# Optimization experiments

Hardware: AMD Instinct MI355X
Metric: run time of the kernel (lower is better)

## Reference

```python
import jax, jax.numpy as jnp
import numpy as np

N_NODES = 50000


def _cluster_gcn_conv(x, row, col, W_out, b_out, W_root, num_nodes):
    # PyG ClusterGCNConv with diag_lambda=0.0 and self-loops already added.
    deg = jax.ops.segment_sum(jnp.ones_like(col, dtype=x.dtype), col,
                              num_segments=num_nodes)
    deg_inv = 1.0 / jnp.clip(deg, 1.0)
    w = deg_inv[col]                       # [E_total]
    msg = x[row] * w[:, None]              # [E_total, d] gather + scale
    agg = jax.ops.segment_sum(msg, col, num_segments=num_nodes)  # scatter-add
    return agg @ W_out + b_out + x @ W_root


def setup_inputs() -> dict:
    key = jax.random.key(0)
    ks = jax.random.split(key, 12)
    N, E, d_in, d_h, d_out = N_NODES, 800000, 128, 128, 64
    x = jax.random.normal(ks[0], (N, d_in), dtype=jnp.float32)
    edge_index = jax.random.randint(ks[1], (2, E), 0, N, dtype=jnp.int64)
    s = lambda fan_in: 1.0 / np.sqrt(fan_in)
    return {
        "x": x,
        "edge_index": edge_index,
        "W1_out": jax.random.normal(ks[2], (d_in, d_h), jnp.float32) * s(d_in),
        "b1": jnp.zeros((d_h,), jnp.float32),
        "W1_root": jax.random.normal(ks[3], (d_in, d_h), jnp.float32) * s(d_in),
        "W2_out": jax.random.normal(ks[4], (d_h, d_h), jnp.float32) * s(d_h),
        "b2": jnp.zeros((d_h,), jnp.float32),
        "W2_root": jax.random.normal(ks[5], (d_h, d_h), jnp.float32) * s(d_h),
        "W3_out": jax.random.normal(ks[6], (d_h, d_out), jnp.float32) * s(d_h),
        "b3": jnp.zeros((d_out,), jnp.float32),
        "W3_root": jax.random.normal(ks[7], (d_h, d_out), jnp.float32) * s(d_h),
    }


def reference(x, edge_index, W1_out, b1, W1_root, W2_out, b2, W2_root,
              W3_out, b3, W3_root):
    N = x.shape[0]
    loops = jnp.arange(N, dtype=edge_index.dtype)
    row = jnp.concatenate([edge_index[0], loops])  # add self loops
    col = jnp.concatenate([edge_index[1], loops])
    # layer 1 + relu (dropout is identity at inference)
    x = jax.nn.relu(_cluster_gcn_conv(x, row, col, W1_out, b1, W1_root, N))
    # layer 2 + relu
    x = jax.nn.relu(_cluster_gcn_conv(x, row, col, W2_out, b2, W2_root, N))
    # layer 3 + relu, then log_softmax (no pooling: node classification)
    x = jax.nn.relu(_cluster_gcn_conv(x, row, col, W3_out, b3, W3_root, N))
    return jax.nn.log_softmax(x, axis=-1)
```

## Files before the change

kernel.cpp:

```cpp
#include <hip/hip_runtime.h>
#include <math.h>


constexpr int DK = 128;
constexpr int NBUCK = 256;
constexpr int ESTRIDE = 3584;

typedef __attribute__((ext_vector_type(8))) short bf16x8;
typedef __attribute__((ext_vector_type(4))) float f32x4;

__device__ inline unsigned short f2bf(float f) {
    unsigned int u; __builtin_memcpy(&u, &f, 4);
    unsigned int r = (u + 0x7FFFu + ((u >> 16) & 1u)) >> 16;
    return (unsigned short)r;
}
__device__ inline float blo(unsigned int u) {
    unsigned int t = u << 16; float f; __builtin_memcpy(&f, &t, 4); return f;
}
__device__ inline float bhi(unsigned int u) {
    unsigned int t = u & 0xffff0000u; float f; __builtin_memcpy(&f, &t, 4); return f;
}

__device__ void wprep_body(const float* __restrict__ Wout, const float* __restrict__ Wroot,
                           uint4* __restrict__ frag, int dout, int tid) {
    int total = 8 * (dout >> 4) * 64;
    if (tid >= total) return;
    int L = tid & 63;
    int fu = (tid >> 6) % (dout >> 4);
    int t = (tid >> 6) / (dout >> 4);
    int quad = L >> 4, l15 = L & 15;
    int n = fu * 16 + l15;
    unsigned int p[4];
#pragma unroll
    for (int jj = 0; jj < 4; ++jj) {
        int k0 = t * 32 + quad * 8 + jj * 2;
        float v0 = (k0 < 128) ? Wout[k0 * dout + n] : Wroot[(k0 - 128) * dout + n];
        int k1 = k0 + 1;
        float v1 = (k1 < 128) ? Wout[k1 * dout + n] : Wroot[(k1 - 128) * dout + n];
        p[jj] = (unsigned)f2bf(v0) | ((unsigned)f2bf(v1) << 16);
    }
    frag[tid] = make_uint4(p[0], p[1], p[2], p[3]);
}

__global__ void k_prep(const float4* __restrict__ x, uint2* __restrict__ xb,
                       const int* __restrict__ row, const int* __restrict__ col,
                       int* __restrict__ bcnt, unsigned int* __restrict__ ebuf,
                       int n4, int E, int bspan,
                       const float* __restrict__ W1o, const float* __restrict__ W1r, uint4* wf1,
                       const float* __restrict__ W2o, const float* __restrict__ W2r, uint4* wf2,
                       const float* __restrict__ W3o, const float* __restrict__ W3r, uint4* wf3) {
    const int nxblk = (n4 + 255) / 256;
    const int b = blockIdx.x;
    const int tid = threadIdx.x;
    if (b < nxblk) {
        int i = b * 256 + tid;
        if (i >= n4) return;
        float4 v = x[i];
        uint2 o;
        o.x = (unsigned)f2bf(v.x) | ((unsigned)f2bf(v.y) << 16);
        o.y = (unsigned)f2bf(v.z) | ((unsigned)f2bf(v.w) << 16);
        xb[i] = o;
    } else if (b < nxblk + 16) {
        wprep_body(W1o, W1r, wf1, 128, (b - nxblk) * 256 + tid);
    } else if (b < nxblk + 32) {
        wprep_body(W2o, W2r, wf2, 128, (b - nxblk - 16) * 256 + tid);
    } else if (b < nxblk + 40) {
        wprep_body(W3o, W3r, wf3, 64, (b - nxblk - 32) * 256 + tid);
    } else {
        __shared__ int cnt[NBUCK];
        __shared__ int base[NBUCK];
        const int t0 = (b - nxblk - 40) * 4096;
        cnt[tid] = 0;
        __syncthreads();
        int bk[16];
#pragma unroll
        for (int k = 0; k < 16; ++k) {
            int i = t0 + k * 256 + tid;
            int bb = -1;
            if (i < E) { bb = col[i] / bspan; atomicAdd(&cnt[bb], 1); }
            bk[k] = bb;
        }
        __syncthreads();
        base[tid] = cnt[tid] ? atomicAdd(&bcnt[tid], cnt[tid]) : 0;
        cnt[tid] = 0;
        __syncthreads();
#pragma unroll
        for (int k = 0; k < 16; ++k) {
            int i = t0 + k * 256 + tid;
            if (i < E) {
                int bb = bk[k];
                int gpos = base[bb] + atomicAdd(&cnt[bb], 1);
                if (gpos < ESTRIDE) {
                    unsigned int colofs = (unsigned)(col[i] - bb * bspan);
                    ebuf[(size_t)bb * ESTRIDE + gpos] =
                        ((unsigned)row[i] & 0xFFFFu) | (colofs << 16);
                }
            }
        }
    }
}

__global__ void k_fillb(const unsigned int* __restrict__ ebuf,
                        const int* __restrict__ bcnt, int* __restrict__ offs,
                        float* __restrict__ deginv, unsigned short* __restrict__ srow,
                        int n, int bspan) {
    __shared__ int cnt[4096];
    __shared__ int scan_s[NBUCK + 1];
    __shared__ int wsum[4];
    const int b = blockIdx.x, tid = threadIdx.x;
    const int lane = tid & 63, wid = tid >> 6;
    {
        int v = min(bcnt[tid], ESTRIDE);
        int ps = v;
#pragma unroll
        for (int off = 1; off < 64; off <<= 1) {
            int t = __shfl_up(ps, off);
            if (lane >= off) ps += t;
        }
        if (lane == 63) wsum[wid] = ps;
        __syncthreads();
        int wb = 0;
        for (int w = 0; w < wid; ++w) wb += wsum[w];
        int excl = wb + ps - v;
        scan_s[tid] = excl;
        if (tid == 255) scan_s[256] = excl + v;
    }
    for (int i = tid; i < 4096; i += 256) cnt[i] = 0;
    __syncthreads();
    const int cntb = min(bcnt[b], ESTRIDE);
    const int csr0 = scan_s[b];
    if (b == NBUCK - 1 && tid == 0) offs[n] = scan_s[256];
    const size_t eb0 = (size_t)b * ESTRIDE;
    for (int i = tid; i < cntb; i += 256) {
        const unsigned u = ebuf[eb0 + i];
        atomicAdd(&cnt[(int)(u >> 16) * 16 + (int)((u & 0xFFFFu) >> 12)], 1);
    }
    __syncthreads();
    int v[16], s = 0;
#pragma unroll
    for (int r = 0; r < 16; ++r) { v[r] = cnt[tid * 16 + r]; s += v[r]; }
    int ps = s;
#pragma unroll
    for (int off = 1; off < 64; off <<= 1) {
        int t = __shfl_up(ps, off);
        if (lane >= off) ps += t;
    }
    if (lane == 63) wsum[wid] = ps;
    __syncthreads();
    int wb = 0;
    for (int w = 0; w < wid; ++w) wb += wsum[w];
    int excl = csr0 + wb + ps - s;
    const int node = b * bspan + tid;
    if (tid < bspan && node < n) {
        offs[node] = excl;
        deginv[node] = 1.0f / (float)(s + 1);
    }
#pragma unroll
    for (int r = 0; r < 16; ++r) { int t = v[r]; cnt[tid * 16 + r] = excl; excl += t; }
    __syncthreads();
    for (int i = tid; i < cntb; i += 256) {
        const unsigned u = ebuf[eb0 + i];
        const int pos = atomicAdd(&cnt[(int)(u >> 16) * 16 + (int)((u & 0xFFFFu) >> 12)], 1);
        srow[pos] = (unsigned short)(u & 0xFFFFu);
    }
}

template <bool HR>
__global__ __launch_bounds__(256, 5)
void k_fused(const unsigned short* __restrict__ xb,
             const int* __restrict__ offs, const unsigned short* __restrict__ srow,
             const float* __restrict__ deginv,
             const uint4* __restrict__ wfrag, const float* __restrict__ bvec,
             unsigned short* __restrict__ y,
             const uint4* __restrict__ wfrag3, const float* __restrict__ b3,
             unsigned short* __restrict__ H, float* __restrict__ R, int n) {
    __shared__ unsigned short At[32][136];
    __shared__ unsigned short sIdx[768];
    const int tid = threadIdx.x;
    const int m0 = blockIdx.x * 32;
    const uint4* __restrict__ xb4 = (const uint4*)xb;

    const int s0 = offs[m0];
    const int eAll = offs[min(m0 + 32, n)];
    const int cntE = eAll - s0;
    const bool staged = (cntE <= 768);
    for (int i = tid; i < cntE && i < 768; i += 256) sIdx[i] = srow[s0 + i];
    __syncthreads();
    const unsigned short* __restrict__ idxp = staged ? sIdx : srow;
    const int bias = staged ? s0 : 0;

#pragma unroll
    for (int rnd = 0; rnd < 2; ++rnd) {
        const int nl = rnd * 16 + (tid >> 4);
        const int lane = tid & 15;
        const int node = m0 + nl;
        if (node < n) {
            const size_t rb = (size_t)node * 16 + lane;
            uint4 sv = xb4[rb];
            float a0 = blo(sv.x), a1 = bhi(sv.x), a2 = blo(sv.y), a3 = bhi(sv.y);
            float a4 = blo(sv.z), a5 = bhi(sv.z), a6 = blo(sv.w), a7 = bhi(sv.w);
            const int s = offs[node] - bias, e = offs[node + 1] - bias;
            int p = s;
            for (; p + 4 <= e; p += 4) {
                const int r0 = idxp[p], r1 = idxp[p + 1];
                const int r2 = idxp[p + 2], r3 = idxp[p + 3];
                const uint4 v0 = xb4[(size_t)r0 * 16 + lane];
                const uint4 v1 = xb4[(size_t)r1 * 16 + lane];
                const uint4 v2 = xb4[(size_t)r2 * 16 + lane];
                const uint4 v3 = xb4[(size_t)r3 * 16 + lane];
                a0 += (blo(v0.x) + blo(v1.x)) + (blo(v2.x) + blo(v3.x));
                a1 += (bhi(v0.x) + bhi(v1.x)) + (bhi(v2.x) + bhi(v3.x));
                a2 += (blo(v0.y) + blo(v1.y)) + (blo(v2.y) + blo(v3.y));
                a3 += (bhi(v0.y) + bhi(v1.y)) + (bhi(v2.y) + bhi(v3.y));
                a4 += (blo(v0.z) + blo(v1.z)) + (blo(v2.z) + blo(v3.z));
                a5 += (bhi(v0.z) + bhi(v1.z)) + (bhi(v2.z) + bhi(v3.z));
                a6 += (blo(v0.w) + blo(v1.w)) + (blo(v2.w) + blo(v3.w));
                a7 += (bhi(v0.w) + bhi(v1.w)) + (bhi(v2.w) + bhi(v3.w));
            }
            for (; p < e; ++p) {
                const uint4 v = xb4[(size_t)idxp[p] * 16 + lane];
                a0 += blo(v.x); a1 += bhi(v.x); a2 += blo(v.y); a3 += bhi(v.y);
                a4 += blo(v.z); a5 += bhi(v.z); a6 += blo(v.w); a7 += bhi(v.w);
            }
            const float w = deginv[node];
            uint4 o;
            o.x = (unsigned)f2bf(a0 * w) | ((unsigned)f2bf(a1 * w) << 16);
            o.y = (unsigned)f2bf(a2 * w) | ((unsigned)f2bf(a3 * w) << 16);
            o.z = (unsigned)f2bf(a4 * w) | ((unsigned)f2bf(a5 * w) << 16);
            o.w = (unsigned)f2bf(a6 * w) | ((unsigned)f2bf(a7 * w) << 16);
            *(uint4*)&At[nl][lane * 8] = o;
        }
    }
    __syncthreads();

    const int w = tid >> 6, L = tid & 63;
    const int quad = L >> 4, l15 = L & 15;

    f32x4 acc[2][2];
#pragma unroll
    for (int mt = 0; mt < 2; ++mt)
#pragma unroll
        for (int u = 0; u < 2; ++u)
            acc[mt][u] = (f32x4){0.f, 0.f, 0.f, 0.f};

    const bf16x8 zf = {0, 0, 0, 0, 0, 0, 0, 0};
#pragma unroll
    for (int t = 0; t < 8; ++t) {
        bf16x8 bfr[2];
#pragma unroll
        for (int u = 0; u < 2; ++u)
            bfr[u] = *(const bf16x8*)&wfrag[(size_t)((t * 8 + (w * 2 + u)) * 64 + L)];
        const int koff = (t & 3) * 32 + quad * 8;
        bf16x8 af[2];
#pragma unroll
        for (int mt = 0; mt < 2; ++mt) {
            const int rl = mt * 16 + l15;
            if (t < 4) {
                af[mt] = *(const bf16x8*)&At[rl][koff];
            } else {
                const int r = m0 + rl;
                af[mt] = (r < n) ? *(const bf16x8*)(xb + (size_t)r * 128 + koff) : zf;
            }
        }
#pragma unroll
        for (int mt = 0; mt < 2; ++mt)
#pragma unroll
            for (int u = 0; u < 2; ++u)
                acc[mt][u] = __builtin_amdgcn_mfma_f32_16x16x32_bf16(
                    af[mt], bfr[u], acc[mt][u], 0, 0, 0);
    }

    float bb[2];
    bb[0] = bvec[w * 32 + l15];
    bb[1] = bvec[w * 32 + 16 + l15];

    if (!HR) {
#pragma unroll
        for (int mt = 0; mt < 2; ++mt)
#pragma unroll
            for (int u = 0; u < 2; ++u)
#pragma unroll
                for (int r4 = 0; r4 < 4; ++r4) {
                    const int r = m0 + mt * 16 + quad * 4 + r4;
                    if (r < n) {
                        float v = fmaxf(acc[mt][u][r4] + bb[u], 0.f);
                        y[(size_t)r * 128 + w * 32 + u * 16 + l15] = f2bf(v);
                    }
                }
        return;
    }

    __syncthreads();
#pragma unroll
    for (int mt = 0; mt < 2; ++mt)
#pragma unroll
        for (int u = 0; u < 2; ++u)
#pragma unroll
            for (int r4 = 0; r4 < 4; ++r4) {
                const int rl = mt * 16 + quad * 4 + r4;
                float v = fmaxf(acc[mt][u][r4] + bb[u], 0.f);
                At[rl][w * 32 + u * 16 + l15] = f2bf(v);
            }
    __syncthreads();

    f32x4 accH[2], accR[2];
#pragma unroll
    for (int mt = 0; mt < 2; ++mt) {
        accH[mt] = (f32x4){0.f, 0.f, 0.f, 0.f};
        accR[mt] = (f32x4){0.f, 0.f, 0.f, 0.f};
    }
#pragma unroll
    for (int t = 0; t < 4; ++t) {
        const bf16x8 bo = *(const bf16x8*)&wfrag3[(size_t)((t * 4 + w) * 64 + L)];
        const bf16x8 br = *(const bf16x8*)&wfrag3[(size_t)(((t + 4) * 4 + w) * 64 + L)];
        const int koff = t * 32 + quad * 8;
        bf16x8 af[2];
#pragma unroll
        for (int mt = 0; mt < 2; ++mt)
            af[mt] = *(const bf16x8*)&At[mt * 16 + l15][koff];
#pragma unroll
        for (int mt = 0; mt < 2; ++mt) {
            accH[mt] = __builtin_amdgcn_mfma_f32_16x16x32_bf16(af[mt], bo, accH[mt], 0, 0, 0);
            accR[mt] = __builtin_amdgcn_mfma_f32_16x16x32_bf16(af[mt], br, accR[mt], 0, 0, 0);
        }
    }
    const float bb3 = b3[w * 16 + l15];
#pragma unroll
    for (int mt = 0; mt < 2; ++mt)
#pragma unroll
        for (int r4 = 0; r4 < 4; ++r4) {
            const int r = m0 + mt * 16 + quad * 4 + r4;
            if (r < n) {
                H[(size_t)r * 64 + w * 16 + l15] = f2bf(accH[mt][r4]);
                R[(size_t)r * 64 + w * 16 + l15] = accR[mt][r4] + bb3;
            }
        }
}

__global__ __launch_bounds__(256, 8)
void k_gather3(const uint2* __restrict__ Hb, const float4* __restrict__ R4,
               const int* __restrict__ offs, const unsigned short* __restrict__ srow,
               const float* __restrict__ deginv, float4* __restrict__ out, int n) {
    __shared__ unsigned short sIdx[512];
    const int tid = threadIdx.x;
    const int m0 = blockIdx.x * 16;
    const int s0 = offs[m0];
    const int eAll = offs[min(m0 + 16, n)];
    const int cntE = eAll - s0;
    const bool staged = (cntE <= 512);
    for (int i = tid; i < cntE && i < 512; i += 256) sIdx[i] = srow[s0 + i];
    __syncthreads();
    const unsigned short* __restrict__ idxp = staged ? sIdx : srow;
    const int bias = staged ? s0 : 0;

    const int node = m0 + (tid >> 4);
    const int lane = tid & 15;
    if (node >= n) return;
    const size_t rb = (size_t)node * 16 + lane;
    uint2 sv = Hb[rb];
    float a0 = blo(sv.x), a1 = bhi(sv.x), a2 = blo(sv.y), a3 = bhi(sv.y);
    const int s = offs[node] - bias, e = offs[node + 1] - bias;
    int p = s;
    for (; p + 4 <= e; p += 4) {
        const int r0 = idxp[p], r1 = idxp[p + 1], r2 = idxp[p + 2], r3 = idxp[p + 3];
        const uint2 v0 = Hb[(size_t)r0 * 16 + lane];
        const uint2 v1 = Hb[(size_t)r1 * 16 + lane];
        const uint2 v2 = Hb[(size_t)r2 * 16 + lane];
        const uint2 v3 = Hb[(size_t)r3 * 16 + lane];
        a0 += (blo(v0.x) + blo(v1.x)) + (blo(v2.x) + blo(v3.x));
        a1 += (bhi(v0.x) + bhi(v1.x)) + (bhi(v2.x) + bhi(v3.x));
        a2 += (blo(v0.y) + blo(v1.y)) + (blo(v2.y) + blo(v3.y));
        a3 += (bhi(v0.y) + bhi(v1.y)) + (bhi(v2.y) + bhi(v3.y));
    }
    for (; p < e; ++p) {
        const uint2 v = Hb[(size_t)idxp[p] * 16 + lane];
        a0 += blo(v.x); a1 += bhi(v.x); a2 += blo(v.y); a3 += bhi(v.y);
    }
    const float w = deginv[node];
    const float4 r = R4[rb];
    float v0 = fmaxf(a0 * w + r.x, 0.f);
    float v1 = fmaxf(a1 * w + r.y, 0.f);
    float v2 = fmaxf(a2 * w + r.z, 0.f);
    float v3 = fmaxf(a3 * w + r.w, 0.f);
    float m = fmaxf(fmaxf(v0, v1), fmaxf(v2, v3));
    m = fmaxf(m, __shfl_xor(m, 1));
    m = fmaxf(m, __shfl_xor(m, 2));
    m = fmaxf(m, __shfl_xor(m, 4));
    m = fmaxf(m, __shfl_xor(m, 8));
    float s2 = __expf(v0 - m) + __expf(v1 - m) + __expf(v2 - m) + __expf(v3 - m);
    s2 += __shfl_xor(s2, 1);
    s2 += __shfl_xor(s2, 2);
    s2 += __shfl_xor(s2, 4);
    s2 += __shfl_xor(s2, 8);
    const float lse = m + __logf(s2);
    out[rb] = make_float4(v0 - lse, v1 - lse, v2 - lse, v3 - lse);
}

extern "C" void kernel_launch(void* const* d_in, const int* in_sizes, int n_in,
                              void* d_out, int out_size, void* d_ws, size_t ws_size,
                              hipStream_t stream) {
    const float* x   = (const float*)d_in[0];
    const int*   ei  = (const int*)d_in[1];
    const float* W1o = (const float*)d_in[2];
    const float* b1  = (const float*)d_in[3];
    const float* W1r = (const float*)d_in[4];
    const float* W2o = (const float*)d_in[5];
    const float* b2  = (const float*)d_in[6];
    const float* W2r = (const float*)d_in[7];
    const float* W3o = (const float*)d_in[8];
    const float* b3  = (const float*)d_in[9];
    const float* W3r = (const float*)d_in[10];

    const int N = in_sizes[0] / DK;
    const int E = in_sizes[1] / 2;
    const int* row = ei;
    const int* col = ei + E;
    const int bspan = (N + NBUCK - 1) / NBUCK;

    int*   bcnt   = (int*)d_ws;
    int*   offs   = bcnt + 256;
    float* deginv = (float*)(offs + ((N + 64) & ~63));
    unsigned short* srow = (unsigned short*)(deginv + ((N + 63) & ~63));
    unsigned int* ebuf = (unsigned int*)(srow + ((E + 63) & ~63));
    uint4* wf1    = (uint4*)(ebuf + (size_t)NBUCK * ESTRIDE);
    uint4* wf2    = wf1 + 4096;
    uint4* wf3    = wf2 + 4096;
    unsigned short* xbuf = (unsigned short*)(wf3 + 2048);
    unsigned short* Ya   = xbuf + (size_t)N * 128;
    unsigned short* Hb   = Ya + (size_t)N * 128;
    float* Rb = (float*)(Hb + (size_t)N * 64);
    float* out = (float*)d_out;

    const int n4 = N * 32;
    const int nxblk = (n4 + 255) / 256;
    const int npart = (E + 4095) / 4096;

    hipMemsetAsync(bcnt, 0, NBUCK * sizeof(int), stream);
    k_prep<<<nxblk + 40 + npart, 256, 0, stream>>>((const float4*)x, (uint2*)xbuf,
                                                   row, col, bcnt, ebuf,
                                                   n4, E, bspan,
                                                   W1o, W1r, wf1, W2o, W2r, wf2,
                                                   W3o, W3r, wf3);
    k_fillb<<<NBUCK, 256, 0, stream>>>(ebuf, bcnt, offs, deginv, srow, N, bspan);

    const int Gf = (N + 31) / 32;
    const int Gg3 = (N + 15) / 16;

    k_fused<false><<<Gf, 256, 0, stream>>>(xbuf, offs, srow, deginv, wf1, b1, Ya,
                                           nullptr, nullptr, nullptr, nullptr, N);
    k_fused<true><<<Gf, 256, 0, stream>>>(Ya, offs, srow, deginv, wf2, b2, nullptr,
                                          wf3, b3, Hb, Rb, N);
    k_gather3<<<Gg3, 256, 0, stream>>>((const uint2*)Hb, (const float4*)Rb,
                                       offs, srow, deginv, (float4*)out, N);
}
```

Measured before the change: 224.6 us.

## Merge all stages into one persistent cooperative kernel with grid syncs

Replaces the memset and five separate kernel launches with a single cooperative persistent kernel. Each phase runs as a grid-stride loop over work units, and grid.sync() separates the phases. Edge partitions become smaller (2048 per block) and are ordered ahead of the x conversion. The aim is to remove launch gaps and memset overhead. In exchange, one shared-memory union and the register budget must fit every phase, which may lower occupancy, and grid-wide barriers plus fewer resident blocks may hurt the latency-bound gather phases.

```diff
diff --git a/kernel.cpp b/kernel.cpp
--- a/kernel.cpp
+++ b/kernel.cpp
@@ -1,10 +1,15 @@
 #include <hip/hip_runtime.h>
+#include <hip/hip_cooperative_groups.h>
 #include <math.h>
+
+namespace cg = cooperative_groups;
 
 
 constexpr int DK = 128;
 constexpr int NBUCK = 256;
 constexpr int ESTRIDE = 3584;
+constexpr int EPB = 2048;
+constexpr int SMEM_BYTES = 17600;
 
 typedef __attribute__((ext_vector_type(8))) short bf16x8;
 typedef __attribute__((ext_vector_type(4))) float f32x4;
@@ -20,6 +25,20 @@
 __device__ inline float bhi(unsigned int u) {
     unsigned int t = u & 0xffff0000u; float f; __builtin_memcpy(&f, &t, 4); return f;
 }
+
+struct KParams {
+    const float4* x; uint2* xb2;
+    const int* row; const int* col;
+    int* bcnt; unsigned int* ebuf;
+    int n4, E, bspan, npart, N;
+    const float *W1o, *W1r, *W2o, *W2r, *W3o, *W3r;
+    uint4 *wf1, *wf2, *wf3;
+    int* offs; float* deginv; unsigned short* srow;
+    const float *b1, *b2, *b3v;
+    unsigned short *xbuf, *Ya, *Hb;
+    float* Rb; float4* out;
+    int phase;
+};
 
 __device__ void wprep_body(const float* __restrict__ Wout, const float* __restrict__ Wroot,
                            uint4* __restrict__ frag, int dout, int tid) {
@@ -42,75 +61,67 @@
     frag[tid] = make_uint4(p[0], p[1], p[2], p[3]);
 }
 
-__global__ void k_prep(const float4* __restrict__ x, uint2* __restrict__ xb,
-                       const int* __restrict__ row, const int* __restrict__ col,
-                       int* __restrict__ bcnt, unsigned int* __restrict__ ebuf,
-                       int n4, int E, int bspan,
-                       const float* __restrict__ W1o, const float* __restrict__ W1r, uint4* wf1,
-                       const float* __restrict__ W2o, const float* __restrict__ W2r, uint4* wf2,
-                       const float* __restrict__ W3o, const float* __restrict__ W3r, uint4* wf3) {
-    const int nxblk = (n4 + 255) / 256;
-    const int b = blockIdx.x;
+__device__ void body_p0(const KParams& P, int u, unsigned char* smem) {
     const int tid = threadIdx.x;
-    if (b < nxblk) {
-        int i = b * 256 + tid;
-        if (i >= n4) return;
-        float4 v = x[i];
-        uint2 o;
-        o.x = (unsigned)f2bf(v.x) | ((unsigned)f2bf(v.y) << 16);
-        o.y = (unsigned)f2bf(v.z) | ((unsigned)f2bf(v.w) << 16);
-        xb[i] = o;
-    } else if (b < nxblk + 16) {
-        wprep_body(W1o, W1r, wf1, 128, (b - nxblk) * 256 + tid);
-    } else if (b < nxblk + 32) {
-        wprep_body(W2o, W2r, wf2, 128, (b - nxblk - 16) * 256 + tid);
-    } else if (b < nxblk + 40) {
-        wprep_body(W3o, W3r, wf3, 64, (b - nxblk - 32) * 256 + tid);
-    } else {
-        __shared__ int cnt[NBUCK];
-        __shared__ int base[NBUCK];
-        const int t0 = (b - nxblk - 40) * 4096;
+    if (u < P.npart) {
+        int* cnt  = (int*)smem;
+        int* base = (int*)(smem + 1024);
+        __syncthreads();
+        const int t0 = u * EPB;
         cnt[tid] = 0;
         __syncthreads();
-        int bk[16];
-#pragma unroll
-        for (int k = 0; k < 16; ++k) {
+        int bk[EPB / 256];
+#pragma unroll
+        for (int k = 0; k < EPB / 256; ++k) {
             int i = t0 + k * 256 + tid;
             int bb = -1;
-            if (i < E) { bb = col[i] / bspan; atomicAdd(&cnt[bb], 1); }
+            if (i < P.E) { bb = P.col[i] / P.bspan; atomicAdd(&cnt[bb], 1); }
             bk[k] = bb;
         }
         __syncthreads();
-        base[tid] = cnt[tid] ? atomicAdd(&bcnt[tid], cnt[tid]) : 0;
+        base[tid] = cnt[tid] ? atomicAdd(&P.bcnt[tid], cnt[tid]) : 0;
         cnt[tid] = 0;
         __syncthreads();
 #pragma unroll
-        for (int k = 0; k < 16; ++k) {
+        for (int k = 0; k < EPB / 256; ++k) {
             int i = t0 + k * 256 + tid;
-            if (i < E) {
+            if (i < P.E) {
                 int bb = bk[k];
                 int gpos = base[bb] + atomicAdd(&cnt[bb], 1);
                 if (gpos < ESTRIDE) {
-                    unsigned int colofs = (unsigned)(col[i] - bb * bspan);
-                    ebuf[(size_t)bb * ESTRIDE + gpos] =
-                        ((unsigned)row[i] & 0xFFFFu) | (colofs << 16);
+                    unsigned int colofs = (unsigned)(P.col[i] - bb * P.bspan);
+                    P.ebuf[(size_t)bb * ESTRIDE + gpos] =
+                        ((unsigned)P.row[i] & 0xFFFFu) | (colofs << 16);
                 }
             }
         }
-    }
-}
-
-__global__ void k_fillb(const unsigned int* __restrict__ ebuf,
-                        const int* __restrict__ bcnt, int* __restrict__ offs,
-                        float* __restrict__ deginv, unsigned short* __restrict__ srow,
-                        int n, int bspan) {
-    __shared__ int cnt[4096];
-    __shared__ int scan_s[NBUCK + 1];
-    __shared__ int wsum[4];
-    const int b = blockIdx.x, tid = threadIdx.x;
+    } else if (u < P.npart + 16) {
+        wprep_body(P.W1o, P.W1r, P.wf1, 128, (u - P.npart) * 256 + tid);
+    } else if (u < P.npart + 32) {
+        wprep_body(P.W2o, P.W2r, P.wf2, 128, (u - P.npart - 16) * 256 + tid);
+    } else if (u < P.npart + 40) {
+        wprep_body(P.W3o, P.W3r, P.wf3, 64, (u - P.npart - 32) * 256 + tid);
+    } else {
+        int i = (u - P.npart - 40) * 256 + tid;
+        if (i < P.n4) {
+            float4 v = P.x[i];
+            uint2 o;
+            o.x = (unsigned)f2bf(v.x) | ((unsigned)f2bf(v.y) << 16);
+            o.y = (unsigned)f2bf(v.z) | ((unsigned)f2bf(v.w) << 16);
+            P.xb2[i] = o;
+        }
+    }
+}
+
+__device__ void body_fillb(const KParams& P, int b, unsigned char* smem) {
+    int* cnt    = (int*)smem;
+    int* scan_s = (int*)(smem + 16384);
+    int* wsum   = (int*)(smem + 17424);
+    const int tid = threadIdx.x;
     const int lane = tid & 63, wid = tid >> 6;
+    __syncthreads();
     {
-        int v = min(bcnt[tid], ESTRIDE);
+        int v = min(P.bcnt[tid], ESTRIDE);
         int ps = v;
 #pragma unroll
         for (int off = 1; off < 64; off <<= 1) {
@@ -127,18 +138,18 @@
     }
     for (int i = tid; i < 4096; i += 256) cnt[i] = 0;
     __syncthreads();
-    const int cntb = min(bcnt[b], ESTRIDE);
+    const int cntb = min(P.bcnt[b], ESTRIDE);
     const int csr0 = scan_s[b];
-    if (b == NBUCK - 1 && tid == 0) offs[n] = scan_s[256];
+    if (b == NBUCK - 1 && tid == 0) P.offs[P.N] = scan_s[256];
     const size_t eb0 = (size_t)b * ESTRIDE;
     for (int i = tid; i < cntb; i += 256) {
-        const unsigned u = ebuf[eb0 + i];
+        const unsigned u = P.ebuf[eb0 + i];
         atomicAdd(&cnt[(int)(u >> 16) * 16 + (int)((u & 0xFFFFu) >> 12)], 1);
     }
     __syncthreads();
-    int v[16], s = 0;
-#pragma unroll
-    for (int r = 0; r < 16; ++r) { v[r] = cnt[tid * 16 + r]; s += v[r]; }
+    int vv[16], s = 0;
+#pragma unroll
+    for (int r = 0; r < 16; ++r) { vv[r] = cnt[tid * 16 + r]; s += vv[r]; }
     int ps = s;
 #pragma unroll
     for (int off = 1; off < 64; off <<= 1) {
@@ -150,43 +161,40 @@
     int wb = 0;
     for (int w = 0; w < wid; ++w) wb += wsum[w];
     int excl = csr0 + wb + ps - s;
-    const int node = b * bspan + tid;
-    if (tid < bspan && node < n) {
-        offs[node] = excl;
-        deginv[node] = 1.0f / (float)(s + 1);
-    }
-#pragma unroll
-    for (int r = 0; r < 16; ++r) { int t = v[r]; cnt[tid * 16 + r] = excl; excl += t; }
+    const int node = b * P.bspan + tid;
+    if (tid < P.bspan && node < P.N) {
+        P.offs[node] = excl;
+        P.deginv[node] = 1.0f / (float)(s + 1);
+    }
+#pragma unroll
+    for (int r = 0; r < 16; ++r) { int t = vv[r]; cnt[tid * 16 + r] = excl; excl += t; }
     __syncthreads();
     for (int i = tid; i < cntb; i += 256) {
-        const unsigned u = ebuf[eb0 + i];
+        const unsigned u = P.ebuf[eb0 + i];
         const int pos = atomicAdd(&cnt[(int)(u >> 16) * 16 + (int)((u & 0xFFFFu) >> 12)], 1);
-        srow[pos] = (unsigned short)(u & 0xFFFFu);
-    }
-}
-
-template <bool HR>
-__global__ __launch_bounds__(256, 5)
-void k_fused(const unsigned short* __restrict__ xb,
-             const int* __restrict__ offs, const unsigned short* __restrict__ srow,
-             const float* __restrict__ deginv,
-             const uint4* __restrict__ wfrag, const float* __restrict__ bvec,
-             unsigned short* __restrict__ y,
-             const uint4* __restrict__ wfrag3, const float* __restrict__ b3,
-             unsigned short* __restrict__ H, float* __restrict__ R, int n) {
-    __shared__ unsigned short At[32][136];
-    __shared__ unsigned short sIdx[768];
+        P.srow[pos] = (unsigned short)(u & 0xFFFFu);
+    }
+}
+
+__device__ void body_fused(const KParams& P, int tb, bool HR, unsigned char* smem) {
+    unsigned short (*At)[136] = (unsigned short (*)[136])smem;
+    unsigned short* sIdx = (unsigned short*)(smem + 8704);
+    const unsigned short* __restrict__ xb = HR ? P.Ya : P.xbuf;
+    const uint4* __restrict__ wfrag = HR ? P.wf2 : P.wf1;
+    const float* __restrict__ bvec = HR ? P.b2 : P.b1;
+    const int n = P.N;
     const int tid = threadIdx.x;
-    const int m0 = blockIdx.x * 32;
+    const int m0 = tb * 32;
     const uint4* __restrict__ xb4 = (const uint4*)xb;
 
-    const int s0 = offs[m0];
-    const int eAll = offs[min(m0 + 32, n)];
+    __syncthreads();
+    const int s0 = P.offs[m0];
+    const int eAll = P.offs[min(m0 + 32, n)];
     const int cntE = eAll - s0;
     const bool staged = (cntE <= 768);
-    for (int i = tid; i < cntE && i < 768; i += 256) sIdx[i] = srow[s0 + i];
-    __syncthreads();
-    const unsigned short* __restrict__ idxp = staged ? sIdx : srow;
+    for (int i = tid; i < cntE && i < 768; i += 256) sIdx[i] = P.srow[s0 + i];
+    __syncthreads();
+    const unsigned short* __restrict__ idxp = staged ? sIdx : P.srow;
     const int bias = staged ? s0 : 0;
 
 #pragma unroll
@@ -199,7 +207,7 @@
             uint4 sv = xb4[rb];
             float a0 = blo(sv.x), a1 = bhi(sv.x), a2 = blo(sv.y), a3 = bhi(sv.y);
             float a4 = blo(sv.z), a5 = bhi(sv.z), a6 = blo(sv.w), a7 = bhi(sv.w);
-            const int s = offs[node] - bias, e = offs[node + 1] - bias;
+            const int s = P.offs[node] - bias, e = P.offs[node + 1] - bias;
             int p = s;
             for (; p + 4 <= e; p += 4) {
                 const int r0 = idxp[p], r1 = idxp[p + 1];
@@ -222,7 +230,7 @@
                 a0 += blo(v.x); a1 += bhi(v.x); a2 += blo(v.y); a3 += bhi(v.y);
                 a4 += blo(v.z); a5 += bhi(v.z); a6 += blo(v.w); a7 += bhi(v.w);
             }
-            const float w = deginv[node];
+            const float w = P.deginv[node];
             uint4 o;
             o.x = (unsigned)f2bf(a0 * w) | ((unsigned)f2bf(a1 * w) << 16);
             o.y = (unsigned)f2bf(a2 * w) | ((unsigned)f2bf(a3 * w) << 16);
@@ -284,116 +292,153 @@
                     const int r = m0 + mt * 16 + quad * 4 + r4;
                     if (r < n) {
                         float v = fmaxf(acc[mt][u][r4] + bb[u], 0.f);
-                        y[(size_t)r * 128 + w * 32 + u * 16 + l15] = f2bf(v);
+                        P.Ya[(size_t)r * 128 + w * 32 + u * 16 + l15] = f2bf(v);
                     }
                 }
-        return;
-    }
-
-    __syncthreads();
-#pragma unroll
-    for (int mt = 0; mt < 2; ++mt)
-#pragma unroll
-        for (int u = 0; u < 2; ++u)
+    } else {
+        __syncthreads();
+#pragma unroll
+        for (int mt = 0; mt < 2; ++mt)
+#pragma unroll
+            for (int u = 0; u < 2; ++u)
+#pragma unroll
+                for (int r4 = 0; r4 < 4; ++r4) {
+                    const int rl = mt * 16 + quad * 4 + r4;
+                    float v = fmaxf(acc[mt][u][r4] + bb[u], 0.f);
+                    At[rl][w * 32 + u * 16 + l15] = f2bf(v);
+                }
+        __syncthreads();
+
+        f32x4 accH[2], accR[2];
+#pragma unroll
+        for (int mt = 0; mt < 2; ++mt) {
+            accH[mt] = (f32x4){0.f, 0.f, 0.f, 0.f};
+            accR[mt] = (f32x4){0.f, 0.f, 0.f, 0.f};
+        }
+#pragma unroll
+        for (int t = 0; t < 4; ++t) {
+            const bf16x8 bo = *(const bf16x8*)&P.wf3[(size_t)((t * 4 + w) * 64 + L)];
+            const bf16x8 br = *(const bf16x8*)&P.wf3[(size_t)(((t + 4) * 4 + w) * 64 + L)];
+            const int koff = t * 32 + quad * 8;
+            bf16x8 af[2];
+#pragma unroll
+            for (int mt = 0; mt < 2; ++mt)
+                af[mt] = *(const bf16x8*)&At[mt * 16 + l15][koff];
+#pragma unroll
+            for (int mt = 0; mt < 2; ++mt) {
+                accH[mt] = __builtin_amdgcn_mfma_f32_16x16x32_bf16(af[mt], bo, accH[mt], 0, 0, 0);
+                accR[mt] = __builtin_amdgcn_mfma_f32_16x16x32_bf16(af[mt], br, accR[mt], 0, 0, 0);
+            }
+        }
+        const float bb3 = P.b3v[w * 16 + l15];
+#pragma unroll
+        for (int mt = 0; mt < 2; ++mt)
 #pragma unroll
             for (int r4 = 0; r4 < 4; ++r4) {
-                const int rl = mt * 16 + quad * 4 + r4;
-                float v = fmaxf(acc[mt][u][r4] + bb[u], 0.f);
-                At[rl][w * 32 + u * 16 + l15] = f2bf(v);
+                const int r = m0 + mt * 16 + quad * 4 + r4;
+                if (r < n) {
+                    P.Hb[(size_t)r * 64 + w * 16 + l15] = f2bf(accH[mt][r4]);
+                    P.Rb[(size_t)r * 64 + w * 16 + l15] = accR[mt][r4] + bb3;
+                }
             }
-    __syncthreads();
-
-    f32x4 accH[2], accR[2];
-#pragma unroll
-    for (int mt = 0; mt < 2; ++mt) {
-        accH[mt] = (f32x4){0.f, 0.f, 0.f, 0.f};
-        accR[mt] = (f32x4){0.f, 0.f, 0.f, 0.f};
-    }
-#pragma unroll
-    for (int t = 0; t < 4; ++t) {
-        const bf16x8 bo = *(const bf16x8*)&wfrag3[(size_t)((t * 4 + w) * 64 + L)];
-        const bf16x8 br = *(const bf16x8*)&wfrag3[(size_t)(((t + 4) * 4 + w) * 64 + L)];
-        const int koff = t * 32 + quad * 8;
-        bf16x8 af[2];
-#pragma unroll
-        for (int mt = 0; mt < 2; ++mt)
-            af[mt] = *(const bf16x8*)&At[mt * 16 + l15][koff];
-#pragma unroll
-        for (int mt = 0; mt < 2; ++mt) {
-            accH[mt] = __builtin_amdgcn_mfma_f32_16x16x32_bf16(af[mt], bo, accH[mt], 0, 0, 0);
-            accR[mt] = __builtin_amdgcn_mfma_f32_16x16x32_bf16(af[mt], br, accR[mt], 0, 0, 0);
-        }
-    }
-    const float bb3 = b3[w * 16 + l15];
-#pragma unroll
-    for (int mt = 0; mt < 2; ++mt)
-#pragma unroll
-        for (int r4 = 0; r4 < 4; ++r4) {
-            const int r = m0 + mt * 16 + quad * 4 + r4;
-            if (r < n) {
-                H[(size_t)r * 64 + w * 16 + l15] = f2bf(accH[mt][r4]);
-                R[(size_t)r * 64 + w * 16 + l15] = accR[mt][r4] + bb3;
-            }
-        }
-}
-
-__global__ __launch_bounds__(256, 8)
-void k_gather3(const uint2* __restrict__ Hb, const float4* __restrict__ R4,
-               const int* __restrict__ offs, const unsigned short* __restrict__ srow,
-               const float* __restrict__ deginv, float4* __restrict__ out, int n) {
-    __shared__ unsigned short sIdx[512];
+    }
+}
+
+__device__ void body_g3(const KParams& P, int tb, unsigned char* smem) {
+    unsigned short* sIdx = (unsigned short*)smem;
     const int tid = threadIdx.x;
-    const int m0 = blockIdx.x * 16;
-    const int s0 = offs[m0];
-    const int eAll = offs[min(m0 + 16, n)];
+    const int m0 = tb * 16;
+    const int n = P.N;
+    const uint2* __restrict__ Hb2 = (const uint2*)P.Hb;
+    const float4* __restrict__ R4 = (const float4*)P.Rb;
+
+    __syncthreads();
+    const int s0 = P.offs[m0];
+    const int eAll = P.offs[min(m0 + 16, n)];
     const int cntE = eAll - s0;
     const bool staged = (cntE <= 512);
-    for (int i = tid; i < cntE && i < 512; i += 256) sIdx[i] = srow[s0 + i];
-    __syncthreads();
-    const unsigned short* __restrict__ idxp = staged ? sIdx : srow;
+    for (int i = tid; i < cntE && i < 512; i += 256) sIdx[i] = P.srow[s0 + i];
+    __syncthreads();
+    const unsigned short* __restrict__ idxp = staged ? sIdx : P.srow;
     const int bias = staged ? s0 : 0;
 
     const int node = m0 + (tid >> 4);
     const int lane = tid & 15;
-    if (node >= n) return;
-    const size_t rb = (size_t)node * 16 + lane;
-    uint2 sv = Hb[rb];
-    float a0 = blo(sv.x), a1 = bhi(sv.x), a2 = blo(sv.y), a3 = bhi(sv.y);
-    const int s = offs[node] - bias, e = offs[node + 1] - bias;
-    int p = s;
-    for (; p + 4 <= e; p += 4) {
-        const int r0 = idxp[p], r1 = idxp[p + 1], r2 = idxp[p + 2], r3 = idxp[p + 3];
-        const uint2 v0 = Hb[(size_t)r0 * 16 + lane];
-        const uint2 v1 = Hb[(size_t)r1 * 16 + lane];
-        const uint2 v2 = Hb[(size_t)r2 * 16 + lane];
-        const uint2 v3 = Hb[(size_t)r3 * 16 + lane];
-        a0 += (blo(v0.x) + blo(v1.x)) + (blo(v2.x) + blo(v3.x));
-        a1 += (bhi(v0.x) + bhi(v1.x)) + (bhi(v2.x) + bhi(v3.x));
-        a2 += (blo(v0.y) + blo(v1.y)) + (blo(v2.y) + blo(v3.y));
-        a3 += (bhi(v0.y) + bhi(v1.y)) + (bhi(v2.y) + bhi(v3.y));
-    }
-    for (; p < e; ++p) {
-        const uint2 v = Hb[(size_t)idxp[p] * 16 + lane];
-        a0 += blo(v.x); a1 += bhi(v.x); a2 += blo(v.y); a3 += bhi(v.y);
-    }
-    const float w = deginv[node];
-    const float4 r = R4[rb];
-    float v0 = fmaxf(a0 * w + r.x, 0.f);
-    float v1 = fmaxf(a1 * w + r.y, 0.f);
-    float v2 = fmaxf(a2 * w + r.z, 0.f);
-    float v3 = fmaxf(a3 * w + r.w, 0.f);
-    float m = fmaxf(fmaxf(v0, v1), fmaxf(v2, v3));
-    m = fmaxf(m, __shfl_xor(m, 1));
-    m = fmaxf(m, __shfl_xor(m, 2));
-    m = fmaxf(m, __shfl_xor(m, 4));
-    m = fmaxf(m, __shfl_xor(m, 8));
-    float s2 = __expf(v0 - m) + __expf(v1 - m) + __expf(v2 - m) + __expf(v3 - m);
-    s2 += __shfl_xor(s2, 1);
-    s2 += __shfl_xor(s2, 2);
-    s2 += __shfl_xor(s2, 4);
-    s2 += __shfl_xor(s2, 8);
-    const float lse = m + __logf(s2);
-    out[rb] = make_float4(v0 - lse, v1 - lse, v2 - lse, v3 - lse);
+    if (node < n) {
+        const size_t rb = (size_t)node * 16 + lane;
+        uint2 sv = Hb2[rb];
+        float a0 = blo(sv.x), a1 = bhi(sv.x), a2 = blo(sv.y), a3 = bhi(sv.y);
+        const int s = P.offs[node] - bias, e = P.offs[node + 1] - bias;
+        int p = s;
+        for (; p + 4 <= e; p += 4) {
+            const int r0 = idxp[p], r1 = idxp[p + 1], r2 = idxp[p + 2], r3 = idxp[p + 3];
+            const uint2 v0 = Hb2[(size_t)r0 * 16 + lane];
+            const uint2 v1 = Hb2[(size_t)r1 * 16 + lane];
+            const uint2 v2 = Hb2[(size_t)r2 * 16 + lane];
+            const uint2 v3 = Hb2[(size_t)r3 * 16 + lane];
+            a0 += (blo(v0.x) + blo(v1.x)) + (blo(v2.x) + blo(v3.x));
+            a1 += (bhi(v0.x) + bhi(v1.x)) + (bhi(v2.x) + bhi(v3.x));
+            a2 += (blo(v0.y) + blo(v1.y)) + (blo(v2.y) + blo(v3.y));
+            a3 += (bhi(v0.y) + bhi(v1.y)) + (bhi(v2.y) + bhi(v3.y));
+        }
+        for (; p < e; ++p) {
+            const uint2 v = Hb2[(size_t)idxp[p] * 16 + lane];
+            a0 += blo(v.x); a1 += bhi(v.x); a2 += blo(v.y); a3 += bhi(v.y);
+        }
+        const float w = P.deginv[node];
+        const float4 r = R4[rb];
+        float v0 = fmaxf(a0 * w + r.x, 0.f);
+        float v1 = fmaxf(a1 * w + r.y, 0.f);
+        float v2 = fmaxf(a2 * w + r.z, 0.f);
+        float v3 = fmaxf(a3 * w + r.w, 0.f);
+        float m = fmaxf(fmaxf(v0, v1), fmaxf(v2, v3));
+        m = fmaxf(m, __shfl_xor(m, 1));
+        m = fmaxf(m, __shfl_xor(m, 2));
+        m = fmaxf(m, __shfl_xor(m, 4));
+        m = fmaxf(m, __shfl_xor(m, 8));
+        float s2 = __expf(v0 - m) + __expf(v1 - m) + __expf(v2 - m) + __expf(v3 - m);
+        s2 += __shfl_xor(s2, 1);
+        s2 += __shfl_xor(s2, 2);
+        s2 += __shfl_xor(s2, 4);
+        s2 += __shfl_xor(s2, 8);
+        const float lse = m + __logf(s2);
+        P.out[rb] = make_float4(v0 - lse, v1 - lse, v2 - lse, v3 - lse);
+    }
+}
+
+__global__ __launch_bounds__(256) void k_all(KParams P) {
+    __shared__ __align__(16) unsigned char smem[SMEM_BYTES];
+    cg::grid_group grid = cg::this_grid();
+    const bool all = (P.phase < 0);
+    const int G = gridDim.x, bid = blockIdx.x;
+    const int tid = threadIdx.x;
+
+    if (all) {
+        if (bid == 0 && tid < NBUCK) P.bcnt[tid] = 0;
+        grid.sync();
+    }
+    if (all || P.phase == 0) {
+        const int U0 = P.npart + 40 + (P.n4 + 255) / 256;
+        for (int u = bid; u < U0; u += G) body_p0(P, u, smem);
+    }
+    if (all) grid.sync();
+    if (all || P.phase == 1) {
+        for (int u = bid; u < NBUCK; u += G) body_fillb(P, u, smem);
+    }
+    if (all) grid.sync();
+    const int Gf = (P.N + 31) / 32;
+    if (all || P.phase == 2) {
+        for (int u = bid; u < Gf; u += G) body_fused(P, u, false, smem);
+    }
+    if (all) grid.sync();
+    if (all || P.phase == 3) {
+        for (int u = bid; u < Gf; u += G) body_fused(P, u, true, smem);
+    }
+    if (all) grid.sync();
+    if (all || P.phase == 4) {
+        const int Gg3 = (P.N + 15) / 16;
+        for (int u = bid; u < Gg3; u += G) body_g3(P, u, smem);
+    }
 }
 
 extern "C" void kernel_launch(void* const* d_in, const int* in_sizes, int n_in,
@@ -401,21 +446,9 @@
                               hipStream_t stream) {
     const float* x   = (const float*)d_in[0];
     const int*   ei  = (const int*)d_in[1];
-    const float* W1o = (const float*)d_in[2];
-    const float* b1  = (const float*)d_in[3];
-    const float* W1r = (const float*)d_in[4];
-    const float* W2o = (const float*)d_in[5];
-    const float* b2  = (const float*)d_in[6];
-    const float* W2r = (const float*)d_in[7];
-    const float* W3o = (const float*)d_in[8];
-    const float* b3  = (const float*)d_in[9];
-    const float* W3r = (const float*)d_in[10];
 
     const int N = in_sizes[0] / DK;
     const int E = in_sizes[1] / 2;
-    const int* row = ei;
-    const int* col = ei + E;
-    const int bspan = (N + NBUCK - 1) / NBUCK;
 
     int*   bcnt   = (int*)d_ws;
     int*   offs   = bcnt + 256;
@@ -429,27 +462,44 @@
     unsigned short* Ya   = xbuf + (size_t)N * 128;
     unsigned short* Hb   = Ya + (size_t)N * 128;
     float* Rb = (float*)(Hb + (size_t)N * 64);
-    float* out = (float*)d_out;
-
-    const int n4 = N * 32;
-    const int nxblk = (n4 + 255) / 256;
-    const int npart = (E + 4095) / 4096;
+
+    KParams P;
+    P.x = (const float4*)x; P.xb2 = (uint2*)xbuf;
+    P.row = ei; P.col = ei + E;
+    P.bcnt = bcnt; P.ebuf = ebuf;
+    P.n4 = N * 32; P.E = E; P.bspan = (N + NBUCK - 1) / NBUCK;
+    P.npart = (E + EPB - 1) / EPB; P.N = N;
+    P.W1o = (const float*)d_in[2];  P.b1 = (const float*)d_in[3];
+    P.W1r = (const float*)d_in[4];
+    P.W2o = (const float*)d_in[5];  P.b2 = (const float*)d_in[6];
+    P.W2r = (const float*)d_in[7];
+    P.W3o = (const float*)d_in[8];  P.b3v = (const float*)d_in[9];
+    P.W3r = (const float*)d_in[10];
+    P.wf1 = wf1; P.wf2 = wf2; P.wf3 = wf3;
+    P.offs = offs; P.deginv = deginv; P.srow = srow;
+    P.xbuf = xbuf; P.Ya = Ya; P.Hb = Hb; P.Rb = Rb;
+    P.out = (float4*)d_out;
+
+    int occ = 0;
+    hipError_t qe = hipOccupancyMaxActiveBlocksPerMultiprocessor(&occ, k_all, 256, 0);
+    if (qe == hipSuccess && occ >= 2) {
+        P.phase = -1;
+        int grid = occ * 256;
+        if (grid > 2048) grid = 2048;
+        void* args[] = { (void*)&P };
+        hipError_t le = hipLaunchCooperativeKernel((const void*)k_all, dim3(grid),
+                                                   dim3(256), args, 0, stream);
+        if (le == hipSuccess) return;
+    }
 
     hipMemsetAsync(bcnt, 0, NBUCK * sizeof(int), stream);
-    k_prep<<<nxblk + 40 + npart, 256, 0, stream>>>((const float4*)x, (uint2*)xbuf,
-                                                   row, col, bcnt, ebuf,
-                                                   n4, E, bspan,
-                                                   W1o, W1r, wf1, W2o, W2r, wf2,
-                                                   W3o, W3r, wf3);
-    k_fillb<<<NBUCK, 256, 0, stream>>>(ebuf, bcnt, offs, deginv, srow, N, bspan);
-
+    const int nxblk = (P.n4 + 255) / 256;
     const int Gf = (N + 31) / 32;
     const int Gg3 = (N + 15) / 16;
-
-    k_fused<false><<<Gf, 256, 0, stream>>>(xbuf, offs, srow, deginv, wf1, b1, Ya,
-                                           nullptr, nullptr, nullptr, nullptr, N);
-    k_fused<true><<<Gf, 256, 0, stream>>>(Ya, offs, srow, deginv, wf2, b2, nullptr,
-                                          wf3, b3, Hb, Rb, N);
-    k_gather3<<<Gg3, 256, 0, stream>>>((const uint2*)Hb, (const float4*)Rb,
-                                       offs, srow, deginv, (float4*)out, N);
-}
+    KParams Q = P;
+    Q.phase = 0; k_all<<<P.npart + 40 + nxblk, 256, 0, stream>>>(Q);
+    Q.phase = 1; k_all<<<NBUCK, 256, 0, stream>>>(Q);
+    Q.phase = 2; k_all<<<Gf, 256, 0, stream>>>(Q);
+    Q.phase = 3; k_all<<<Gf, 256, 0, stream>>>(Q);
+    Q.phase = 4; k_all<<<Gg3, 256, 0, stream>>>(Q);
+}
```

After: 256.2 us. +14.1%, slower.
